# Kernel tuning notes

Hardware: AMD Instinct MI355X
Metric: run time of the kernel (lower is better)

The kernel has to match this reference:

```python
import jax, jax.numpy as jnp
import numpy as np

B, H, D, SIZE, S = 32, 16, 64, 262144, 1024
GAMMA = 0.99

def setup_inputs() -> dict:
    key = jax.random.key(0)
    k1, k2, k3, k4 = jax.random.split(key, 4)
    return {
        "query": jax.random.normal(k1, (B, H, D), jnp.float32),
        "key_store": jax.random.normal(k2, (SIZE, H, D), jnp.float32),
        "value_store": jax.random.normal(k3, (SIZE, H, D), jnp.float32),
        "logit_store": 0.1 * jax.random.normal(k4, (SIZE, H), jnp.float32),
    }

def _sample_indices(logit_store, batch, rng):
    # torch softmax over dim=0 (batch*head rows) => per-row weights over s are
    # w[s] proportional to exp(logit[s,h]) / sum_h' exp(logit[s,h'])
    logw = logit_store.T - jax.nn.logsumexp(logit_store, axis=1)[None, :]  # (H, SIZE)
    u = jax.random.uniform(rng, (batch,) + logw.shape, minval=1e-12, maxval=1.0)
    gumbel = -jnp.log(-jnp.log(u))
    # Gumbel top-k == sampling without replacement proportional to exp(logw)
    _, idx = jax.lax.top_k(logw[None] + gumbel, S)  # (B, H, S)
    return idx

def reference(query, key_store, value_store, logit_store):
    b, h, d = query.shape
    idx = _sample_indices(logit_store, b, jax.random.key(42))  # (B,H,S)
    hidx = jnp.arange(h)[None, :, None]  # (1,H,1) broadcasts against idx
    kst = key_store.transpose(1, 0, 2)   # (H, SIZE, D)
    vst = value_store.transpose(1, 0, 2)
    sk = kst[hidx, idx]  # (B,H,S,D) gathered sample keys
    sv = vst[hidx, idx]  # (B,H,S,D) gathered sample values
    attn = jax.nn.softmax(jnp.einsum('bhd,bhsd->bhs', query, sk) * (d ** -0.5), axis=-1)
    lerp_k = jnp.einsum('bhs,bhsd->bhd', attn, sk)
    lerp_v = jnp.einsum('bhs,bhsd->bhd', attn, sv)
    # scattered in-place store updates
    new_k = (1.0 - attn)[..., None] * sk + attn[..., None] * lerp_k[:, :, None, :]
    new_v = (1.0 - attn)[..., None] * sv + attn[..., None] * lerp_v[:, :, None, :]
    key_store_new = kst.at[hidx, idx].set(new_k).transpose(1, 0, 2)
    value_store_new = vst.at[hidx, idx].set(new_v).transpose(1, 0, 2)
    lst = logit_store.T  # (H, SIZE)
    new_l = GAMMA * lst[hidx, idx] + attn  # RHS uses gathered old logits (matches torch)
    logit_store_new = lst.at[hidx, idx].set(new_l).T
    return lerp_k, lerp_v, key_store_new, value_store_new, logit_store_new
```

## Files before the change

### kernel.cpp

```cpp
#include <hip/hip_runtime.h>
#include <stdint.h>

static constexpr int NB = 32, NH = 16, ND = 64, NS = 1024;
static constexpr int SZ = 262144;
static constexpr int NROW = NB * NH;
static constexpr long N4 = 67108864L;
static constexpr long HALF4 = 33554432L;
static constexpr int SPLIT_IDX = 131072;

typedef float f32x4 __attribute__((ext_vector_type(4)));

__device__ __forceinline__ uint32_t rotl32(uint32_t x, int r) { return (x << r) | (x >> (32 - r)); }

__device__ __forceinline__ void tf2x32(uint32_t x0, uint32_t x1, uint32_t& o0, uint32_t& o1) {
  const uint32_t K1 = 42u, K2 = 0x1BD11BF0u;
  x1 += K1;
#define TFR(r) { x0 += x1; x1 = rotl32(x1, (r)); x1 ^= x0; }
  TFR(13) TFR(15) TFR(26) TFR(6)
  x0 += K1; x1 += K2 + 1u;
  TFR(17) TFR(29) TFR(16) TFR(24)
  x0 += K2; x1 += 2u;
  TFR(13) TFR(15) TFR(26) TFR(6)
  x1 += K1 + 3u;
  TFR(17) TFR(29) TFR(16) TFR(24)
  x0 += K1; x1 += K2 + 4u;
  TFR(13) TFR(15) TFR(26) TFR(6)
  x0 += K2; x1 += 5u;
#undef TFR
  o0 = x0; o1 = x1;
}

__device__ __forceinline__ uint32_t bits_of(uint32_t row, uint32_t s) {
  uint32_t o0, o1; tf2x32(0u, (row << 18) | s, o0, o1);
  return o0 ^ o1;
}

__device__ __forceinline__ float gumbel_precise(uint32_t row, uint32_t s) {
  uint32_t bits = bits_of(row, s);
  float f = __uint_as_float((bits >> 9) | 0x3f800000u) - 1.0f;
  float u = fmaxf(1e-12f, f + 1e-12f);
  float t = -logf(u);
  return -logf(t);
}

__device__ __forceinline__ float uf_of(uint32_t row, uint32_t s) {
  return __uint_as_float((bits_of(row, s) >> 9) | 0x3f800000u);
}

__device__ __forceinline__ uint32_t fkey(float v) {
  uint32_t u = __float_as_uint(v);
  return (u & 0x80000000u) ? ~u : (u | 0x80000000u);
}

__global__ void k_logw(const float* __restrict__ logit, float* __restrict__ logw,
                       float* __restrict__ wexp, float* __restrict__ outL,
                       int* __restrict__ winner, float* __restrict__ W) {
  __shared__ float sW[16];
  const int tid = threadIdx.x;
  if (tid < 16) sW[tid] = 0.f;
  __syncthreads();
  int s = blockIdx.x * 256 + tid;
  const float4* p = (const float4*)(logit + (size_t)s * NH);
  float4 a0 = p[0], a1 = p[1], a2 = p[2], a3 = p[3];
  float x[16] = {a0.x,a0.y,a0.z,a0.w, a1.x,a1.y,a1.z,a1.w,
                 a2.x,a2.y,a2.z,a2.w, a3.x,a3.y,a3.z,a3.w};
  float m = x[0];
#pragma unroll
  for (int h = 1; h < 16; ++h) m = fmaxf(m, x[h]);
  float acc = 0.f;
#pragma unroll
  for (int h = 0; h < 16; ++h) acc += expf(x[h] - m);
  float lse = logf(acc) + m;
  float wl[16];
#pragma unroll
  for (int h = 0; h < 16; ++h) {
    float lw = x[h] - lse;
    logw[(size_t)h * SZ + s] = lw;
    float e = expf(lw);
    wexp[(size_t)h * SZ + s] = e;
    wl[h] = e;
  }
#pragma unroll
  for (int h = 0; h < 16; ++h) {
    float v = wl[h];
#pragma unroll
    for (int off = 32; off; off >>= 1) v += __shfl_xor(v, off);
    if ((tid & 63) == 0) atomicAdd(&sW[h], v);
  }
  float4* q = (float4*)(outL + (size_t)s * NH);
  q[0] = a0; q[1] = a1; q[2] = a2; q[3] = a3;
  int4 mone = make_int4(-1, -1, -1, -1);
  int4* w = (int4*)(winner + (size_t)s * NH);
  w[0] = mone; w[1] = mone; w[2] = mone; w[3] = mone;
  __syncthreads();
  if (tid < 16) atomicAdd(&W[tid], sW[tid]);
}

__device__ __forceinline__ void find_thresh(const uint32_t* hist, int nbins, int chunk,
                                            uint32_t need, int* outT, int tid) {
  if (tid < 64) {
    int hi = nbins - 1 - tid * chunk;
    uint32_t csum = 0;
    for (int j = 0; j < chunk; ++j) csum += hist[hi - j];
    uint32_t inc = csum;
#pragma unroll
    for (int off = 1; off < 64; off <<= 1) {
      uint32_t t = (uint32_t)__shfl_up((int)inc, off);
      if (tid >= off) inc += t;
    }
    uint32_t pre = inc - csum;
    if (pre < need && inc >= need) {
      uint32_t cum = pre; int T = hi - chunk + 1;
      for (int j = 0; j < chunk; ++j) {
        int b = hi - j;
        if (cum + hist[b] >= need) { T = b; break; }
        cum += hist[b];
      }
      *outT = T;
    }
  }
}

#define MEGA_T 512
#define SEL_BLKS 512
#define COPY_BLKS 2048
#define NCAND 5120
__global__ void __launch_bounds__(MEGA_T, 8) k_mega(
    const float* __restrict__ logw, const float* __restrict__ wexp,
    const float* __restrict__ Wsum, const float* __restrict__ qin,
    const float* __restrict__ Kst, const float* __restrict__ Vst,
    int* __restrict__ idx_sel, float* __restrict__ attn_ws,
    float* __restrict__ lerp_k, float* __restrict__ lerp_v, int* __restrict__ winner,
    f32x4* __restrict__ oK4, f32x4* __restrict__ oV4) {
  const int bid = blockIdx.x;
  const int tid = threadIdx.x;

  if (bid >= SEL_BLKS) {
    const f32x4* K4 = (const f32x4*)Kst;
    const f32x4* V4 = (const f32x4*)Vst;
    const long base = (long)(bid - SEL_BLKS) * MEGA_T + tid;
    const long stride = (long)COPY_BLKS * MEGA_T;
    for (int r = 0; r < 8; ++r) {
      long i0 = base + (long)(4 * r) * stride;
      long i1 = i0 + stride, i2 = i0 + 2 * stride, i3 = i0 + 3 * stride;
      f32x4 k0 = __builtin_nontemporal_load(&K4[i0]);
      f32x4 k1 = __builtin_nontemporal_load(&K4[i1]);
      f32x4 k2 = __builtin_nontemporal_load(&K4[i2]);
      f32x4 k3 = __builtin_nontemporal_load(&K4[i3]);
      f32x4 v0 = __builtin_nontemporal_load(&V4[i0]);
      f32x4 v1 = __builtin_nontemporal_load(&V4[i1]);
      f32x4 v2 = __builtin_nontemporal_load(&V4[i2]);
      f32x4 v3 = __builtin_nontemporal_load(&V4[i3]);
      __builtin_nontemporal_store(k0, &oK4[i0]);
      __builtin_nontemporal_store(k1, &oK4[i1]);
      __builtin_nontemporal_store(k2, &oK4[i2]);
      __builtin_nontemporal_store(k3, &oK4[i3]);
      __builtin_nontemporal_store(v0, &oV4[i0]);
      __builtin_nontemporal_store(v1, &oV4[i1]);
      __builtin_nontemporal_store(v2, &oV4[i2]);
      __builtin_nontemporal_store(v3, &oV4[i3]);
    }
    return;
  }

  const int row = bid;
  const int h = row & 15, b = row >> 4;
  const float* lw = logw + (size_t)h * SZ;
  const f32x4* we4 = (const f32x4*)(wexp + (size_t)h * SZ);
  int* outrow = idx_sel + (size_t)row * NS;

  __shared__ union {
    struct {
      int      cidx[NCAND];
      uint32_t hist[2048];
      uint16_t candA[2048];
      uint16_t candB[256];
      uint16_t candC[64];
    } s;
    struct {
      int   sel_s[NS];
      float sc[NS];
      float red[MEGA_T];
      f32x4 pk4[8][16], pv4[8][16];
    } a;
  } u;
  __shared__ int ctl[8];
  __shared__ float sNB;

  if (tid == 0) {
    float Wh = Wsum[h];
    sNB = -4096.0f / Wh;
    ctl[1] = 0;
  }
  __syncthreads();
  const float nB = sNB;
  const float CThr = 1.9999996f;

  for (int g = tid; g < SZ / 4; g += MEGA_T) {
    f32x4 w4 = we4[g];
    int s0 = g << 2;
    float u0 = uf_of(row, s0);
    float u1 = uf_of(row, s0 + 1);
    float u2 = uf_of(row, s0 + 2);
    float u3 = uf_of(row, s0 + 3);
    if (u0 >= fmaf(nB, w4.x, CThr)) { int p = atomicAdd(&ctl[1], 1); if (p < NCAND) u.s.cidx[p] = s0; }
    if (u1 >= fmaf(nB, w4.y, CThr)) { int p = atomicAdd(&ctl[1], 1); if (p < NCAND) u.s.cidx[p] = s0 + 1; }
    if (u2 >= fmaf(nB, w4.z, CThr)) { int p = atomicAdd(&ctl[1], 1); if (p < NCAND) u.s.cidx[p] = s0 + 2; }
    if (u3 >= fmaf(nB, w4.w, CThr)) { int p = atomicAdd(&ctl[1], 1); if (p < NCAND) u.s.cidx[p] = s0 + 3; }
  }
  __syncthreads();
  const int C = min(ctl[1], NCAND);

  for (int i = tid; i < 2048; i += MEGA_T) u.s.hist[i] = 0;
  if (tid == 0) { ctl[0] = 0; ctl[3] = 0; ctl[4] = 0; ctl[5] = 0; }
  __syncthreads();
  for (int ci = tid; ci < C; ci += MEGA_T) {
    int s = u.s.cidx[ci];
    uint32_t k = fkey(lw[s] + gumbel_precise(row, s));
    atomicAdd(&u.s.hist[k >> 21], 1u);
  }
  __syncthreads();
  find_thresh(u.s.hist, 2048, 32, (uint32_t)NS, &ctl[2], tid);
  __syncthreads();
  const int T0 = ctl[2];
  for (int ci = tid; ci < C; ci += MEGA_T) {
    int s = u.s.cidx[ci];
    uint32_t k = fkey(lw[s] + gumbel_precise(row, s));
    int bb = (int)(k >> 21);
    if (bb > T0)       { int p = atomicAdd(&ctl[0], 1); outrow[p] = s; }
    else if (bb == T0) { int c = atomicAdd(&ctl[3], 1); if (c < 2048) u.s.candA[c] = (uint16_t)ci; }
  }
  __syncthreads();
  const int CA = min(ctl[3], 2048);
  for (int i = tid; i < 2048; i += MEGA_T) u.s.hist[i] = 0;
  __syncthreads();
  for (int i = tid; i < CA; i += MEGA_T) {
    int s = u.s.cidx[u.s.candA[i]];
    uint32_t k = fkey(lw[s] + gumbel_precise(row, s));
    atomicAdd(&u.s.hist[(k >> 10) & 0x7FFu], 1u);
  }
  __syncthreads();
  find_thresh(u.s.hist, 2048, 32, (uint32_t)(NS - ctl[0]), &ctl[2], tid);
  __syncthreads();
  const int T1 = ctl[2];
  for (int i = tid; i < CA; i += MEGA_T) {
    int ci = u.s.candA[i];
    int s = u.s.cidx[ci];
    uint32_t k = fkey(lw[s] + gumbel_precise(row, s));
    int mid = (int)((k >> 10) & 0x7FFu);
    if (mid > T1)       { int p = atomicAdd(&ctl[0], 1); outrow[p] = s; }
    else if (mid == T1) { int c = atomicAdd(&ctl[4], 1); if (c < 256) u.s.candB[c] = (uint16_t)ci; }
  }
  __syncthreads();
  const int CB = min(ctl[4], 256);
  for (int i = tid; i < 1024; i += MEGA_T) u.s.hist[i] = 0;
  __syncthreads();
  for (int i = tid; i < CB; i += MEGA_T) {
    int s = u.s.cidx[u.s.candB[i]];
    uint32_t k = fkey(lw[s] + gumbel_precise(row, s));
    atomicAdd(&u.s.hist[k & 0x3FFu], 1u);
  }
  __syncthreads();
  find_thresh(u.s.hist, 1024, 16, (uint32_t)(NS - ctl[0]), &ctl[2], tid);
  __syncthreads();
  const int T2 = ctl[2];
  for (int i = tid; i < CB; i += MEGA_T) {
    int ci = u.s.candB[i];
    int s = u.s.cidx[ci];
    uint32_t k = fkey(lw[s] + gumbel_precise(row, s));
    int lo = (int)(k & 0x3FFu);
    if (lo > T2)       { int p = atomicAdd(&ctl[0], 1); outrow[p] = s; }
    else if (lo == T2) { int c = atomicAdd(&ctl[5], 1); if (c < 64) u.s.candC[c] = (uint16_t)ci; }
  }
  __syncthreads();
  if (tid == 0) {
    int need = NS - ctl[0];
    int cc = min(ctl[5], 64);
    for (int k = 0; k < need; ++k) {
      int best = 0x7fffffff, bi = 0;
      for (int j = 0; j < cc; ++j) { int s = u.s.cidx[u.s.candC[j]]; if (s < best) { best = s; bi = j; } }
      if (best == 0x7fffffff) best = 0;
      outrow[ctl[0] + k] = best;
      if (cc > 0) u.s.cidx[u.s.candC[bi]] = 0x7fffffff;
    }
  }
  __syncthreads();

  const f32x4* K4 = (const f32x4*)Kst;
  const f32x4* V4 = (const f32x4*)Vst;
  const int lane = tid & 63, wv = tid >> 6;
  const int sj = lane >> 3, dj = lane & 7;
  for (int i = tid; i < NS; i += MEGA_T) u.a.sel_s[i] = outrow[i];
  const f32x4* q4 = (const f32x4*)(qin + (size_t)row * ND);
  f32x4 qa = q4[dj * 2], qb = q4[dj * 2 + 1];
  __syncthreads();
  for (int it = 0; it < 16; it += 2) {
    int i1 = it * 64 + wv * 8 + sj;
    int i2 = i1 + 64;
    int x1 = u.a.sel_s[i1], x2 = u.a.sel_s[i2];
    size_t b1 = ((size_t)x1 * NH + h) * 16 + dj * 2;
    size_t b2 = ((size_t)x2 * NH + h) * 16 + dj * 2;
    f32x4 ka1 = K4[b1], kb1 = K4[b1 + 1];
    f32x4 ka2 = K4[b2], kb2 = K4[b2 + 1];
    float p1 = ka1.x*qa.x + ka1.y*qa.y + ka1.z*qa.z + ka1.w*qa.w
             + kb1.x*qb.x + kb1.y*qb.y + kb1.z*qb.z + kb1.w*qb.w;
    float p2 = ka2.x*qa.x + ka2.y*qa.y + ka2.z*qa.z + ka2.w*qa.w
             + kb2.x*qb.x + kb2.y*qb.y + kb2.z*qb.z + kb2.w*qb.w;
#pragma unroll
    for (int off = 1; off < 8; off <<= 1) { p1 += __shfl_xor(p1, off); p2 += __shfl_xor(p2, off); }
    if (dj == 0) { u.a.sc[i1] = p1 * 0.125f; u.a.sc[i2] = p2 * 0.125f; }
  }
  __syncthreads();
  float v1 = u.a.sc[tid], v2 = u.a.sc[tid + 512];
  u.a.red[tid] = fmaxf(v1, v2); __syncthreads();
  for (int s = 256; s; s >>= 1) { if (tid < s) u.a.red[tid] = fmaxf(u.a.red[tid], u.a.red[tid + s]); __syncthreads(); }
  float m = u.a.red[0]; __syncthreads();
  float e1 = expf(v1 - m), e2 = expf(v2 - m);
  u.a.red[tid] = e1 + e2; __syncthreads();
  for (int s = 256; s; s >>= 1) { if (tid < s) u.a.red[tid] += u.a.red[tid + s]; __syncthreads(); }
  float inv = 1.0f / u.a.red[0];
  float a1 = e1 * inv, a2 = e2 * inv;
  u.a.sc[tid] = a1; u.a.sc[tid + 512] = a2;
  attn_ws[(size_t)row * NS + tid] = a1;
  attn_ws[(size_t)row * NS + tid + 512] = a2;
  __syncthreads();
  f32x4 AK = 0.f, BK = 0.f, AV = 0.f, BV = 0.f;
  for (int it = 0; it < 16; it += 2) {
    int i1 = it * 64 + wv * 8 + sj;
    int i2 = i1 + 64;
    int x1 = u.a.sel_s[i1], x2 = u.a.sel_s[i2];
    float c1 = u.a.sc[i1], c2 = u.a.sc[i2];
    size_t b1 = ((size_t)x1 * NH + h) * 16 + dj * 2;
    size_t b2 = ((size_t)x2 * NH + h) * 16 + dj * 2;
    f32x4 k1a = K4[b1], k1b = K4[b1 + 1], v1a = V4[b1], v1b = V4[b1 + 1];
    f32x4 k2a = K4[b2], k2b = K4[b2 + 1], v2a = V4[b2], v2b = V4[b2 + 1];
    AK += c1 * k1a + c2 * k2a; BK += c1 * k1b + c2 * k2b;
    AV += c1 * v1a + c2 * v2a; BV += c1 * v1b + c2 * v2b;
  }
#pragma unroll
  for (int off = 8; off < 64; off <<= 1) {
    AK.x += __shfl_xor(AK.x, off); AK.y += __shfl_xor(AK.y, off);
    AK.z += __shfl_xor(AK.z, off); AK.w += __shfl_xor(AK.w, off);
    BK.x += __shfl_xor(BK.x, off); BK.y += __shfl_xor(BK.y, off);
    BK.z += __shfl_xor(BK.z, off); BK.w += __shfl_xor(BK.w, off);
    AV.x += __shfl_xor(AV.x, off); AV.y += __shfl_xor(AV.y, off);
    AV.z += __shfl_xor(AV.z, off); AV.w += __shfl_xor(AV.w, off);
    BV.x += __shfl_xor(BV.x, off); BV.y += __shfl_xor(BV.y, off);
    BV.z += __shfl_xor(BV.z, off); BV.w += __shfl_xor(BV.w, off);
  }
  if (sj == 0) {
    u.a.pk4[wv][dj * 2] = AK; u.a.pk4[wv][dj * 2 + 1] = BK;
    u.a.pv4[wv][dj * 2] = AV; u.a.pv4[wv][dj * 2 + 1] = BV;
  }
  __syncthreads();
  if (tid < 64) {
    float lk = 0.f, lv = 0.f;
    const float* pkf = (const float*)u.a.pk4;
    const float* pvf = (const float*)u.a.pv4;
#pragma unroll
    for (int ww = 0; ww < 8; ++ww) { lk += pkf[ww * 64 + tid]; lv += pvf[ww * 64 + tid]; }
    lerp_k[(size_t)row * ND + tid] = lk;
    lerp_v[(size_t)row * ND + tid] = lv;
  }
  for (int i = tid; i < NS; i += MEGA_T) atomicMax(&winner[(size_t)u.a.sel_s[i] * NH + h], b);
}

__global__ void k_mark(const int* __restrict__ idx_sel, const float* __restrict__ attn_ws,
                       const int* __restrict__ winner, const float* __restrict__ Lst,
                       float* __restrict__ wa, float* __restrict__ outL) {
  int t = blockIdx.x * 256 + threadIdx.x;
  int row = t >> 10, h = row & 15, b = row >> 4;
  int idx = idx_sel[t];
  size_t slot = (size_t)idx * NH + h;
  if (winner[slot] == b) {
    float a = attn_ws[t];
    wa[slot] = a;
    outL[slot] = 0.99f * Lst[slot] + a;
  }
}

#define TAIL_COPY_BLKS 4096
__global__ void __launch_bounds__(256) k_tail(const f32x4* __restrict__ K4,
    const f32x4* __restrict__ V4, const int* __restrict__ winner,
    const float* __restrict__ wa, const f32x4* __restrict__ LK4,
    const f32x4* __restrict__ LV4, const int* __restrict__ idx_sel,
    const float* __restrict__ attn_ws, f32x4* __restrict__ oK4, f32x4* __restrict__ oV4) {
  const int bid = blockIdx.x;
  if (bid < TAIL_COPY_BLKS) {
    const long base = HALF4 + (long)bid * 256 + threadIdx.x;
    const long stride = (long)TAIL_COPY_BLKS * 256;
    for (int r = 0; r < 8; ++r) {
      long i0 = base + (long)(4 * r) * stride;
      long i1 = i0 + stride, i2 = i0 + 2 * stride, i3 = i0 + 3 * stride;
      int s0 = (int)(i0 >> 4), s1 = (int)(i1 >> 4), s2 = (int)(i2 >> 4), s3 = (int)(i3 >> 4);
      int w0 = winner[s0], w1 = winner[s1], w2 = winner[s2], w3 = winner[s3];
      f32x4 k0 = __builtin_nontemporal_load(&K4[i0]);
      f32x4 k1 = __builtin_nontemporal_load(&K4[i1]);
      f32x4 k2 = __builtin_nontemporal_load(&K4[i2]);
      f32x4 k3 = __builtin_nontemporal_load(&K4[i3]);
      f32x4 v0 = __builtin_nontemporal_load(&V4[i0]);
      f32x4 v1 = __builtin_nontemporal_load(&V4[i1]);
      f32x4 v2 = __builtin_nontemporal_load(&V4[i2]);
      f32x4 v3 = __builtin_nontemporal_load(&V4[i3]);
      if (w0 >= 0) {
        float a = wa[s0]; int rr = (w0 << 4) | (s0 & 15); float o = 1.0f - a;
        k0 = o * k0 + a * LK4[((long)rr << 4) + (i0 & 15)];
        v0 = o * v0 + a * LV4[((long)rr << 4) + (i0 & 15)];
      }
      if (w1 >= 0) {
        float a = wa[s1]; int rr = (w1 << 4) | (s1 & 15); float o = 1.0f - a;
        k1 = o * k1 + a * LK4[((long)rr << 4) + (i1 & 15)];
        v1 = o * v1 + a * LV4[((long)rr << 4) + (i1 & 15)];
      }
      if (w2 >= 0) {
        float a = wa[s2]; int rr = (w2 << 4) | (s2 & 15); float o = 1.0f - a;
        k2 = o * k2 + a * LK4[((long)rr << 4) + (i2 & 15)];
        v2 = o * v2 + a * LV4[((long)rr << 4) + (i2 & 15)];
      }
      if (w3 >= 0) {
        float a = wa[s3]; int rr = (w3 << 4) | (s3 & 15); float o = 1.0f - a;
        k3 = o * k3 + a * LK4[((long)rr << 4) + (i3 & 15)];
        v3 = o * v3 + a * LV4[((long)rr << 4) + (i3 & 15)];
      }
      __builtin_nontemporal_store(k0, &oK4[i0]);
      __builtin_nontemporal_store(k1, &oK4[i1]);
      __builtin_nontemporal_store(k2, &oK4[i2]);
      __builtin_nontemporal_store(k3, &oK4[i3]);
      __builtin_nontemporal_store(v0, &oV4[i0]);
      __builtin_nontemporal_store(v1, &oV4[i1]);
      __builtin_nontemporal_store(v2, &oV4[i2]);
      __builtin_nontemporal_store(v3, &oV4[i3]);
    }
    return;
  }
  int g = (bid - TAIL_COPY_BLKS) * 4 + (threadIdx.x >> 6);
  int lane = threadIdx.x & 63;
  int row = g >> 10, i = g & 1023;
  int h = row & 15, b = row >> 4;
  int idx = idx_sel[(size_t)row * NS + i];
  if (idx >= SPLIT_IDX) return;
  size_t slot = (size_t)idx * NH + h;
  if (winner[slot] != b) return;
  float a = attn_ws[(size_t)row * NS + i];
  size_t base = slot * (size_t)ND + lane;
  float kv = ((const float*)K4)[base], vv = ((const float*)V4)[base];
  float lk = ((const float*)LK4)[(size_t)row * ND + lane];
  float lv = ((const float*)LV4)[(size_t)row * ND + lane];
  float o = 1.0f - a;
  ((float*)oK4)[base] = o * kv + a * lk;
  ((float*)oV4)[base] = o * vv + a * lv;
}

extern "C" void kernel_launch(void* const* d_in, const int* in_sizes, int n_in,
                              void* d_out, int out_size, void* d_ws, size_t ws_size,
                              hipStream_t stream) {
  const float* q   = (const float*)d_in[0];
  const float* Kst = (const float*)d_in[1];
  const float* Vst = (const float*)d_in[2];
  const float* Lst = (const float*)d_in[3];

  float* out    = (float*)d_out;
  float* out_lk = out;
  float* out_lv = out + 32768;
  float* outK   = out + 65536;
  float* outV   = outK + 268435456;
  float* outL   = outV + 268435456;

  char* ws = (char*)d_ws;
  float* logw   = (float*)ws;
  float* wexp   = (float*)(ws + (16ull << 20));
  int*   idxsel = (int*)(ws + (32ull << 20));
  float* attn   = (float*)(ws + (34ull << 20));
  int*   winner = (int*)(ws + (36ull << 20));
  float* wa     = (float*)(ws + (52ull << 20));
  float* Wsum   = (float*)(ws + (68ull << 20));

  hipMemsetAsync(Wsum, 0, 16 * sizeof(float), stream);
  k_logw<<<SZ / 256, 256, 0, stream>>>(Lst, logw, wexp, outL, winner, Wsum);
  k_mega<<<SEL_BLKS + COPY_BLKS, MEGA_T, 0, stream>>>(logw, wexp, Wsum, q, Kst, Vst,
                                                      idxsel, attn, out_lk, out_lv, winner,
                                                      (f32x4*)outK, (f32x4*)outV);
  k_mark<<<NROW * NS / 256, 256, 0, stream>>>(idxsel, attn, winner, Lst, wa, outL);
  k_tail<<<TAIL_COPY_BLKS + NROW * NS / 4, 256, 0, stream>>>(
      (const f32x4*)Kst, (const f32x4*)Vst, winner, wa,
      (const f32x4*)out_lk, (const f32x4*)out_lv, idxsel, attn,
      (f32x4*)outK, (f32x4*)outV);
}
```

Before: 1.172 ms.

## Split candidate filtering into separate kernel with two blocks per row

Moves the per-row Gumbel candidate prefilter out of the mega kernel into a new k_filter kernel that uses two blocks per row, each scanning half of the index range and writing candidates to global workspace. The finish kernel then loads these candidates instead of scanning all 262144 entries itself. This doubles parallelism for the RNG-heavy filter pass and shortens the selection blocks that previously ran alongside the copy blocks. In exchange it adds a kernel launch, a global round trip for the candidates, and it no longer overlaps the filter work with the store copy in the same launch.

```diff
diff --git a/kernel.cpp b/kernel.cpp
--- a/kernel.cpp
+++ b/kernel.cpp
@@ -96,6 +96,43 @@
   if (tid < 16) atomicAdd(&W[tid], sW[tid]);
 }
 
+#define FILT_T 512
+#define HCAP 4096
+__global__ void __launch_bounds__(FILT_T, 8) k_filter(
+    const float* __restrict__ wexp, const float* __restrict__ Wsum,
+    int* __restrict__ gcand, int* __restrict__ gcnt) {
+  const int bid = blockIdx.x;
+  const int tid = threadIdx.x;
+  const int row = bid >> 1, half = bid & 1;
+  const int h = row & 15;
+  const f32x4* we4 = (const f32x4*)(wexp + (size_t)h * SZ);
+  __shared__ int cidx[HCAP];
+  __shared__ int scnt;
+  __shared__ float sNB;
+  if (tid == 0) { scnt = 0; sNB = -4096.0f / Wsum[h]; }
+  __syncthreads();
+  const float nB = sNB;
+  const float CThr = 1.9999996f;
+  const int gbase = half * (SZ / 8);
+  for (int g = gbase + tid; g < gbase + SZ / 8; g += FILT_T) {
+    f32x4 w4 = we4[g];
+    int s0 = g << 2;
+    float u0 = uf_of(row, s0);
+    float u1 = uf_of(row, s0 + 1);
+    float u2 = uf_of(row, s0 + 2);
+    float u3 = uf_of(row, s0 + 3);
+    if (u0 >= fmaf(nB, w4.x, CThr)) { int p = atomicAdd(&scnt, 1); if (p < HCAP) cidx[p] = s0; }
+    if (u1 >= fmaf(nB, w4.y, CThr)) { int p = atomicAdd(&scnt, 1); if (p < HCAP) cidx[p] = s0 + 1; }
+    if (u2 >= fmaf(nB, w4.z, CThr)) { int p = atomicAdd(&scnt, 1); if (p < HCAP) cidx[p] = s0 + 2; }
+    if (u3 >= fmaf(nB, w4.w, CThr)) { int p = atomicAdd(&scnt, 1); if (p < HCAP) cidx[p] = s0 + 3; }
+  }
+  __syncthreads();
+  int c = min(scnt, HCAP);
+  int* dst = gcand + (size_t)row * (2 * HCAP) + half * HCAP;
+  for (int i = tid; i < c; i += FILT_T) dst[i] = cidx[i];
+  if (tid == 0) gcnt[bid] = c;
+}
+
 __device__ __forceinline__ void find_thresh(const uint32_t* hist, int nbins, int chunk,
                                             uint32_t need, int* outT, int tid) {
   if (tid < 64) {
@@ -124,10 +161,10 @@
 #define MEGA_T 512
 #define SEL_BLKS 512
 #define COPY_BLKS 2048
-#define NCAND 5120
-__global__ void __launch_bounds__(MEGA_T, 8) k_mega(
-    const float* __restrict__ logw, const float* __restrict__ wexp,
-    const float* __restrict__ Wsum, const float* __restrict__ qin,
+#define NCAND 6144
+__global__ void __launch_bounds__(MEGA_T, 8) k_finish(
+    const float* __restrict__ logw, const int* __restrict__ gcand,
+    const int* __restrict__ gcnt, const float* __restrict__ qin,
     const float* __restrict__ Kst, const float* __restrict__ Vst,
     int* __restrict__ idx_sel, float* __restrict__ attn_ws,
     float* __restrict__ lerp_k, float* __restrict__ lerp_v, int* __restrict__ winner,
@@ -166,7 +203,6 @@
   const int row = bid;
   const int h = row & 15, b = row >> 4;
   const float* lw = logw + (size_t)h * SZ;
-  const f32x4* we4 = (const f32x4*)(wexp + (size_t)h * SZ);
   int* outrow = idx_sel + (size_t)row * NS;
 
   __shared__ union {
@@ -185,35 +221,18 @@
     } a;
   } u;
   __shared__ int ctl[8];
-  __shared__ float sNB;
-
-  if (tid == 0) {
-    float Wh = Wsum[h];
-    sNB = -4096.0f / Wh;
-    ctl[1] = 0;
-  }
-  __syncthreads();
-  const float nB = sNB;
-  const float CThr = 1.9999996f;
-
-  for (int g = tid; g < SZ / 4; g += MEGA_T) {
-    f32x4 w4 = we4[g];
-    int s0 = g << 2;
-    float u0 = uf_of(row, s0);
-    float u1 = uf_of(row, s0 + 1);
-    float u2 = uf_of(row, s0 + 2);
-    float u3 = uf_of(row, s0 + 3);
-    if (u0 >= fmaf(nB, w4.x, CThr)) { int p = atomicAdd(&ctl[1], 1); if (p < NCAND) u.s.cidx[p] = s0; }
-    if (u1 >= fmaf(nB, w4.y, CThr)) { int p = atomicAdd(&ctl[1], 1); if (p < NCAND) u.s.cidx[p] = s0 + 1; }
-    if (u2 >= fmaf(nB, w4.z, CThr)) { int p = atomicAdd(&ctl[1], 1); if (p < NCAND) u.s.cidx[p] = s0 + 2; }
-    if (u3 >= fmaf(nB, w4.w, CThr)) { int p = atomicAdd(&ctl[1], 1); if (p < NCAND) u.s.cidx[p] = s0 + 3; }
-  }
-  __syncthreads();
-  const int C = min(ctl[1], NCAND);
-
+
+  const int c0 = min(gcnt[row * 2], HCAP);
+  int c1 = min(gcnt[row * 2 + 1], HCAP);
+  if (c0 + c1 > NCAND) c1 = NCAND - c0;
+  const int* src = gcand + (size_t)row * (2 * HCAP);
+  for (int i = tid; i < c0; i += MEGA_T) u.s.cidx[i] = src[i];
+  for (int i = tid; i < c1; i += MEGA_T) u.s.cidx[c0 + i] = src[HCAP + i];
+  if (tid == 0) { ctl[0] = 0; ctl[3] = 0; ctl[4] = 0; ctl[5] = 0; }
   for (int i = tid; i < 2048; i += MEGA_T) u.s.hist[i] = 0;
-  if (tid == 0) { ctl[0] = 0; ctl[3] = 0; ctl[4] = 0; ctl[5] = 0; }
-  __syncthreads();
+  __syncthreads();
+  const int C = c0 + c1;
+
   for (int ci = tid; ci < C; ci += MEGA_T) {
     int s = u.s.cidx[ci];
     uint32_t k = fkey(lw[s] + gumbel_precise(row, s));
@@ -473,13 +492,16 @@
   float* attn   = (float*)(ws + (34ull << 20));
   int*   winner = (int*)(ws + (36ull << 20));
   float* wa     = (float*)(ws + (52ull << 20));
-  float* Wsum   = (float*)(ws + (68ull << 20));
+  int*   gcand  = (int*)(ws + (68ull << 20));
+  int*   gcnt   = (int*)(ws + (84ull << 20));
+  float* Wsum   = (float*)(ws + (84ull << 20) + 8192);
 
   hipMemsetAsync(Wsum, 0, 16 * sizeof(float), stream);
   k_logw<<<SZ / 256, 256, 0, stream>>>(Lst, logw, wexp, outL, winner, Wsum);
-  k_mega<<<SEL_BLKS + COPY_BLKS, MEGA_T, 0, stream>>>(logw, wexp, Wsum, q, Kst, Vst,
-                                                      idxsel, attn, out_lk, out_lv, winner,
-                                                      (f32x4*)outK, (f32x4*)outV);
+  k_filter<<<2 * NROW, FILT_T, 0, stream>>>(wexp, Wsum, gcand, gcnt);
+  k_finish<<<SEL_BLKS + COPY_BLKS, MEGA_T, 0, stream>>>(logw, gcand, gcnt, q, Kst, Vst,
+                                                        idxsel, attn, out_lk, out_lv, winner,
+                                                        (f32x4*)outK, (f32x4*)outV);
   k_mark<<<NROW * NS / 256, 256, 0, stream>>>(idxsel, attn, winner, Lst, wa, outL);
   k_tail<<<TAIL_COPY_BLKS + NROW * NS / 4, 256, 0, stream>>>(
       (const f32x4*)Kst, (const f32x4*)Vst, winner, wa,
```

Result: slower. 1.433 ms (+22.3%).
